# Performance work log

Hardware: AMD Instinct MI355X
Metric: run time of the kernel (lower is better)

The kernel has to match this reference:

```python
import jax, jax.numpy as jnp
import numpy as np

B, L, HID = 2, 2048, 512
NUM_HEADS = 8
HEAD_DIM = HID // NUM_HEADS
GAP_ROWS = 33   # num_time_gap_buckets + 1
DUR_ROWS = 17   # num_duration_buckets + 1
NEG = -1e9      # finite stand-in for -inf (grad-safe, masked probs ~0)


def setup_inputs() -> dict:
    key = jax.random.key(0)
    ks = jax.random.split(key, 16)
    s = 1.0 / np.sqrt(HID)
    x = jax.random.normal(ks[0], (B, L, HID), dtype=jnp.float32)
    attention_mask = jax.random.randint(ks[1], (B, L), 0, 2, dtype=jnp.int32)
    time_gap_bucket_ids = jax.random.randint(ks[2], (B, L), 0, GAP_ROWS, dtype=jnp.int32)
    duration_bucket_ids = jax.random.randint(ks[3], (B, L), 0, DUR_ROWS, dtype=jnp.int32)
    Wq = jax.random.normal(ks[4], (HID, HID), dtype=jnp.float32) * s
    bq = jnp.zeros((HID,), jnp.float32)
    Wk = jax.random.normal(ks[5], (HID, HID), dtype=jnp.float32) * s
    bk = jnp.zeros((HID,), jnp.float32)
    Wv = jax.random.normal(ks[6], (HID, HID), dtype=jnp.float32) * s
    bv = jnp.zeros((HID,), jnp.float32)
    Wo = jax.random.normal(ks[7], (HID, HID), dtype=jnp.float32) * s
    bo = jnp.zeros((HID,), jnp.float32)
    # bias tables: padding_idx=0 row kept at zero, rest random for a meaningful test
    gap_emb = jax.random.normal(ks[8], (GAP_ROWS, NUM_HEADS), dtype=jnp.float32) * 0.1
    gap_emb = gap_emb.at[0].set(0.0)
    dur_emb = jax.random.normal(ks[9], (DUR_ROWS, NUM_HEADS), dtype=jnp.float32) * 0.1
    dur_emb = dur_emb.at[0].set(0.0)
    return dict(x=x, attention_mask=attention_mask,
                time_gap_bucket_ids=time_gap_bucket_ids,
                duration_bucket_ids=duration_bucket_ids,
                Wq=Wq, bq=bq, Wk=Wk, bk=bk, Wv=Wv, bv=bv, Wo=Wo, bo=bo,
                gap_emb=gap_emb, dur_emb=dur_emb)


def reference(x, attention_mask, time_gap_bucket_ids, duration_bucket_ids,
              Wq, bq, Wk, bk, Wv, bv, Wo, bo, gap_emb, dur_emb):
    b, l, hid = x.shape
    h, d = NUM_HEADS, HEAD_DIM
    def split_heads(t):  # (B,L,HID) -> (B,h,L,d)
        return t.reshape(b, l, h, d).transpose(0, 2, 1, 3)
    Q = split_heads(x @ Wq + bq)
    K = split_heads(x @ Wk + bk)
    V = split_heads(x @ Wv + bv)
    scores = jnp.einsum('bhqd,bhkd->bhqk', Q, K) / jnp.sqrt(jnp.float32(d))
    # relative time-gap bias: (B,L,L) bucket lookup -> (B,h,L,L)
    rel = jnp.abs(time_gap_bucket_ids[:, :, None] - time_gap_bucket_ids[:, None, :])
    rel = jnp.clip(rel, 0, GAP_ROWS - 1)
    gap_bias = gap_emb[rel]                       # (B,L,L,h)
    scores = scores + gap_bias.transpose(0, 3, 1, 2)
    # per-key duration bias: (B,L,h) -> (B,h,1,L)
    dur_bias = dur_emb[duration_bucket_ids]       # (B,L,h)
    scores = scores + dur_bias.transpose(0, 2, 1)[:, :, None, :]
    pad = (attention_mask == 0)[:, None, None, :]  # (B,1,1,L) over keys
    scores = jnp.where(pad, NEG, scores)
    attn = jax.nn.softmax(scores, axis=-1)
    out = jnp.einsum('bhqk,bhkd->bhqd', attn, V)
    out = out.transpose(0, 2, 1, 3).reshape(b, l, hid)
    return out @ Wo + bo
```

## Files before the change

### kernel.cpp

```cpp
#include <hip/hip_runtime.h>
#include <cmath>

typedef unsigned short u16;
typedef unsigned int   u32;
typedef __attribute__((ext_vector_type(2))) unsigned uintx2;
typedef __attribute__((ext_vector_type(4))) float    floatx4;
typedef __attribute__((ext_vector_type(4))) unsigned uintx4;
typedef __attribute__((ext_vector_type(8))) __bf16   bf16x8;

#define MFMA16(a, b, c) __builtin_amdgcn_mfma_f32_16x16x32_bf16((a), (b), (c), 0, 0, 0)

__device__ __forceinline__ u16 f2bf(float f) {
    union { float f; u32 u; } v; v.f = f;
    u32 u = v.u;
    return (u16)((u + 0x7FFFu + ((u >> 16) & 1u)) >> 16);
}

__device__ __forceinline__ bf16x8 ld_frag(const u16* p) {
    uintx4 t = *(const uintx4*)p;
    return __builtin_bit_cast(bf16x8, t);
}

#if __has_builtin(__builtin_amdgcn_exp2f)
#define EXP2F(x) __builtin_amdgcn_exp2f(x)
#else
#define EXP2F(x) exp2f(x)
#endif

typedef __attribute__((address_space(3))) unsigned       lds_u32;
typedef __attribute__((address_space(1))) const unsigned glb_u32;
__device__ __forceinline__ void gl_lds16(const void* g, void* l) {
    __builtin_amdgcn_global_load_lds((glb_u32*)(uintptr_t)g, (lds_u32*)(uintptr_t)l, 16, 0, 0);
}

#define DRAIN() asm volatile("s_waitcnt vmcnt(0)" ::: "memory")

#define LOG2E   1.4426950408889634f
#define QSCALE  0.18033688011112043f

__global__ __launch_bounds__(256) void prep_kernel(
        const float* __restrict__ x, const int* __restrict__ gap_ids,
        const int* __restrict__ dur_ids, const int* __restrict__ amask,
        const float* __restrict__ gap_emb, const float* __restrict__ dur_emb,
        const float* __restrict__ Wq, const float* __restrict__ Wk,
        const float* __restrict__ Wv, const float* __restrict__ Wo,
        u16* __restrict__ Xb, u16* __restrict__ Qe, u16* __restrict__ Ke,
        u16* __restrict__ WqT, u16* __restrict__ WkT,
        u16* __restrict__ WvT, u16* __restrict__ WoT) {
    __shared__ u16 T[64][72];
    int bid = blockIdx.x, tid = threadIdx.x;
    if (bid < 1024) {
        int idx = bid * 256 + tid;
        const float* src = x + (size_t)idx * 8;
        uintx4 o;
        o.x = f2bf(src[0]) | ((u32)f2bf(src[1]) << 16);
        o.y = f2bf(src[2]) | ((u32)f2bf(src[3]) << 16);
        o.z = f2bf(src[4]) | ((u32)f2bf(src[5]) << 16);
        o.w = f2bf(src[6]) | ((u32)f2bf(src[7]) << 16);
        *(uintx4*)(Xb + (size_t)idx * 8) = o;
    } else if (bid < 2048) {
        int ri = (bid - 1024) * 32 + (tid >> 3);
        int l = ri & 2047;
        int b = ri >> 14;
        int ch = tid & 7;
        int gq = gap_ids[b * 2048 + l];
        u16 lg = f2bf(LOG2E);
        u16 vals[8];
        for (int e = 0; e < 8; e++) {
            int j = ch * 8 + e;
            vals[e] = (j == gq || j == 33) ? lg : (u16)0;
        }
        *(uintx4*)(Qe + (size_t)ri * 128 + (8 + ch) * 8) = *(uintx4*)vals;
    } else if (bid < 3072) {
        int ri = (bid - 2048) * 32 + (tid >> 3);
        int bh = ri >> 11, l = ri & 2047;
        int b = bh >> 3, h = bh & 7;
        int ch = tid & 7;
        int gk = gap_ids[b * 2048 + l];
        int did = dur_ids[b * 2048 + l];
        int msk = amask[b * 2048 + l];
        float kval = msk ? dur_emb[did * 8 + h] : -1e9f;
        u16 vals[8];
        for (int e = 0; e < 8; e++) {
            int j = ch * 8 + e;
            float v;
            if (j <= 32) { int d = j - gk; d = d < 0 ? -d : d; v = gap_emb[d * 8 + h]; }
            else if (j == 33) v = kval;
            else v = 0.f;
            vals[e] = f2bf(v);
        }
        int phys = 8 | (ch ^ (l & 7));
        *(uintx4*)(Ke + (size_t)ri * 128 + phys * 8) = *(uintx4*)vals;
    } else {
        int bid2 = bid - 3072;
        int mat = bid2 >> 6, t8 = bid2 & 63;
        int n0 = (t8 & 7) * 64, k0 = (t8 >> 3) * 64;
        const float* W = (mat == 0) ? Wq : (mat == 1) ? Wk : (mat == 2) ? Wv : Wo;
        u16* WT = (mat == 0) ? WqT : (mat == 1) ? WkT : (mat == 2) ? WvT : WoT;
        int r = tid >> 4, cq = tid & 15;
        for (int rr = 0; rr < 4; rr++) {
            int row = r + rr * 16;
            floatx4 s = *(const floatx4*)&W[(size_t)(k0 + row) * 512 + n0 + cq * 4];
            T[cq * 4 + 0][row] = f2bf(s.x);
            T[cq * 4 + 1][row] = f2bf(s.y);
            T[cq * 4 + 2][row] = f2bf(s.z);
            T[cq * 4 + 3][row] = f2bf(s.w);
        }
        __syncthreads();
        for (int p = 0; p < 2; p++) {
            int idx = p * 256 + tid;
            int c = idx >> 3, ch = idx & 7;
            *(uintx4*)&WT[(size_t)(n0 + c) * 512 + k0 + ch * 8] = *(const uintx4*)&T[c][ch * 8];
        }
    }
}

__global__ __launch_bounds__(256) void gemm_qkv(
        const u16* __restrict__ Xb,
        const u16* __restrict__ WqT, const u16* __restrict__ WkT, const u16* __restrict__ WvT,
        const float* __restrict__ bq, const float* __restrict__ bk, const float* __restrict__ bv,
        u16* __restrict__ Qe, u16* __restrict__ Ke, u16* __restrict__ Vt) {
    __shared__ u16 smem[2][12288];

    int tid = threadIdx.x;
    int m0 = blockIdx.x * 128;
    int gy = blockIdx.y;
    int mat = gy >> 3, hh = gy & 7;
    int ncol0 = hh * 64;
    const u16* Bt = (mat == 0) ? WqT : (mat == 1) ? WkT : WvT;
    const float* bias = (mat == 0) ? bq : (mat == 1) ? bk : bv;

    int lane = tid & 63, w = tid >> 6, lo = lane & 15, hi = lane >> 4;
    int wm = w >> 1, wn = w & 1;
    floatx4 acc[4][2] = {};

#define QSTAGE(KB, BUF) do {                                                            \
        int k0_ = (KB) * 64;                                                            \
        for (int it = 0; it < 4; it++) {                                                \
            int c = it * 256 + tid;                                                     \
            int row = c >> 3, ch = c & 7;                                               \
            gl_lds16((const char*)Xb + ((size_t)(m0 + row) * 512 + k0_) * 2 + ch * 16,  \
                     (char*)(smem[BUF]) + c * 16);                                      \
        }                                                                               \
        for (int it = 0; it < 2; it++) {                                                \
            int c = it * 256 + tid;                                                     \
            int row = c >> 3, ch = c & 7;                                               \
            gl_lds16((const char*)Bt + ((size_t)(ncol0 + row) * 512 + k0_) * 2 + ch * 16,\
                     (char*)(smem[BUF] + 8192) + c * 16);                               \
        }                                                                               \
    } while (0)

    QSTAGE(0, 0);
    for (int kb = 0; kb < 8; kb++) {
        DRAIN();
        __syncthreads();
        if (kb + 1 < 8) QSTAGE(kb + 1, (kb + 1) & 1);
        const u16* As = smem[kb & 1];
        const u16* Bs = smem[kb & 1] + 8192;
        for (int s = 0; s < 2; s++) {
            bf16x8 a[4], b[2];
            for (int i = 0; i < 4; i++)
                a[i] = ld_frag(&As[(64 * wm + 16 * i + lo) * 64 + s * 32 + hi * 8]);
            for (int j = 0; j < 2; j++)
                b[j] = ld_frag(&Bs[(32 * wn + 16 * j + lo) * 64 + s * 32 + hi * 8]);
            for (int i = 0; i < 4; i++)
                for (int j = 0; j < 2; j++)
                    acc[i][j] = MFMA16(a[i], b[j], acc[i][j]);
        }
    }
#undef QSTAGE

    int bb = m0 >> 11, l0 = m0 & 2047;
    __syncthreads();

    if (mat < 2) {
        u16* Ot = smem[0];
        for (int j = 0; j < 2; j++) {
            int col = 32 * wn + 16 * j + lo;
            float bval = bias[ncol0 + col];
            for (int i = 0; i < 4; i++) {
                int row = 64 * wm + 16 * i + 4 * hi;
                for (int r = 0; r < 4; r++) {
                    float v = acc[i][j][r] + bval;
                    if (mat == 0) v *= QSCALE;
                    Ot[(row + r) * 72 + col] = f2bf(v);
                }
            }
        }
        __syncthreads();
        for (int p = 0; p < 4; p++) {
            int cc = p * 256 + tid;
            int row = cc >> 3, ch = cc & 7;
            int lrow = l0 + row;
            size_t rowi = (size_t)(bb * 8 + hh) * 2048 + lrow;
            int ch2 = (mat == 1) ? (ch ^ (lrow & 7)) : ch;
            u16* dstp = (mat == 0) ? Qe : Ke;
            *(uintx4*)(dstp + rowi * 128 + ch2 * 8) = *(const uintx4*)(Ot + row * 72 + ch * 8);
        }
    } else {
        u16* Ot = smem[0];
        for (int j = 0; j < 2; j++) {
            int dc = 32 * wn + 16 * j + lo;
            float bval = bias[ncol0 + dc];
            for (int i = 0; i < 4; i++) {
                int row = 64 * wm + 16 * i + 4 * hi;
                for (int r = 0; r < 4; r++)
                    Ot[dc * 136 + row + r] = f2bf(acc[i][j][r] + bval);
            }
        }
        __syncthreads();
        for (int p = 0; p < 4; p++) {
            int cc4 = p * 256 + tid;
            int dc = cc4 >> 4, c16 = cc4 & 15;
            int g64 = c16 >> 3, phys = c16 & 7;
            int mlog = phys ^ (dc & 7);
            int g = mlog >> 2, q = mlog & 3;
            int base = g64 * 64 + 32 * g + 4 * q;
            uintx2 lo4 = *(const uintx2*)(Ot + dc * 136 + base);
            uintx2 hi4 = *(const uintx2*)(Ot + dc * 136 + base + 16);
            uintx4 t; t.x = lo4.x; t.y = lo4.y; t.z = hi4.x; t.w = hi4.y;
            size_t dst = ((size_t)(bb * 8 + hh) * 64 + dc) * 2048 + l0 + g64 * 64 + phys * 8;
            *(uintx4*)(Vt + dst) = t;
        }
    }
}

__global__ __launch_bounds__(256, 3) void flash_attn(
        const u16* __restrict__ Qe, const u16* __restrict__ Ke, const u16* __restrict__ Vt,
        float* __restrict__ Opart, float* __restrict__ Lpart) {
    __shared__ u16 Ks[2][64 * 128];
    __shared__ u16 Vs[2][64 * 64];

    int tid = threadIdx.x, lane = tid & 63, w = tid >> 6, lo = lane & 15, hi = lane >> 4;
    int qt2 = blockIdx.x, bh = blockIdx.y, sp = blockIdx.z;
    int sw = lo & 7;

    bf16x8 bq_[2][4];
    for (int g = 0; g < 2; g++) {
        size_t qrow = ((size_t)bh * 2048 + qt2 * 128 + g * 64 + 16 * w + lo) * 128;
        for (int kc = 0; kc < 4; kc++) bq_[g][kc] = ld_frag(&Qe[qrow + kc * 32 + hi * 8]);
    }

    floatx4 O[2][4] = {};
    floatx4 Lacc[2] = {};
    uintx4 onesu; onesu.x = 0x3F803F80u; onesu.y = 0x3F803F80u; onesu.z = 0x3F803F80u; onesu.w = 0x3F803F80u;
    bf16x8 ones = __builtin_bit_cast(bf16x8, onesu);

    const u16* KeB = Ke + (size_t)bh * 2048 * 128;
    const u16* VtB = Vt + (size_t)bh * 64 * 2048;

    int kbeg = sp * 16, kend = kbeg + 16;

#define STAGE(KT, BUF) do {                                                        \
        int k0_ = (KT) * 64;                                                       \
        const char* gk_ = (const char*)(KeB + (size_t)k0_ * 128);                  \
        char* lk_ = (char*)Ks[BUF];                                                \
        for (int r2 = 0; r2 < 4; r2++)                                             \
            gl_lds16(gk_ + r2 * 4096 + tid * 16, lk_ + r2 * 4096 + tid * 16);      \
        for (int p2 = 0; p2 < 2; p2++) {                                           \
            int c_ = p2 * 256 + tid;                                               \
            int row_ = c_ >> 3, ch_ = c_ & 7;                                      \
            gl_lds16((const char*)(VtB + (size_t)row_ * 2048 + k0_) + ch_ * 16,    \
                     (char*)Vs[BUF] + c_ * 16);                                    \
        }                                                                          \
    } while (0)

    int cur = 0;
    STAGE(kbeg, 0);
    for (int kt = kbeg; kt < kend; kt++) {
        DRAIN();
        __syncthreads();
        if (kt + 1 < kend) STAGE(kt + 1, cur ^ 1);

        const u16* Ksc = Ks[cur];
        const u16* Vsc = Vs[cur];

        floatx4 sf[2][4] = {};
        for (int t = 0; t < 4; t++) {
            const u16* krow = &Ksc[(16 * t + lo) * 128];
            for (int kc = 0; kc < 4; kc++) {
                int cc = kc * 4 + hi;
                int pc = (cc & 8) | ((cc & 7) ^ sw);
                bf16x8 a = ld_frag(&krow[pc * 8]);
                sf[0][t] = MFMA16(a, bq_[0][kc], sf[0][t]);
                sf[1][t] = MFMA16(a, bq_[1][kc], sf[1][t]);
            }
        }

        bf16x8 af[2][2];
        for (int g = 0; g < 2; g++) {
            u32 pk[4][2];
            for (int t = 0; t < 4; t++) {
                float p0 = EXP2F(sf[g][t][0]);
                float p1 = EXP2F(sf[g][t][1]);
                float p2 = EXP2F(sf[g][t][2]);
                float p3 = EXP2F(sf[g][t][3]);
                u32 u0 = __builtin_bit_cast(u32, p0) + 0x8000u;
                u32 u1 = __builtin_bit_cast(u32, p1) + 0x8000u;
                u32 u2 = __builtin_bit_cast(u32, p2) + 0x8000u;
                u32 u3 = __builtin_bit_cast(u32, p3) + 0x8000u;
                pk[t][0] = __builtin_amdgcn_perm(u1, u0, 0x07060302);
                pk[t][1] = __builtin_amdgcn_perm(u3, u2, 0x07060302);
            }
            for (int tp = 0; tp < 2; tp++) {
                uintx4 av;
                av.x = pk[2 * tp][0]; av.y = pk[2 * tp][1];
                av.z = pk[2 * tp + 1][0]; av.w = pk[2 * tp + 1][1];
                af[g][tp] = __builtin_bit_cast(bf16x8, av);
            }
        }

        for (int tp = 0; tp < 2; tp++) {
            Lacc[0] = MFMA16(af[0][tp], ones, Lacc[0]);
            Lacc[1] = MFMA16(af[1][tp], ones, Lacc[1]);
            for (int u = 0; u < 4; u++) {
                const u16* vrow = &Vsc[(16 * u + lo) * 64];
                int m = (4 * tp + hi) ^ sw;
                bf16x8 bv = ld_frag(&vrow[m * 8]);
                O[0][u] = MFMA16(af[0][tp], bv, O[0][u]);
                O[1][u] = MFMA16(af[1][tp], bv, O[1][u]);
            }
        }
        cur ^= 1;
    }
#undef STAGE

    for (int g = 0; g < 2; g++) {
        int qt = 2 * qt2 + g;
        size_t obase = (((size_t)sp * 16 + bh) * 32 + qt) * 4096;
        for (int u = 0; u < 4; u++)
            for (int r = 0; r < 4; r++)
                Opart[obase + (size_t)(16 * w + 4 * hi + r) * 64 + 16 * u + lo] = O[g][u][r];
        if (lo == 0) {
            size_t lbase = (((size_t)sp * 16 + bh) * 32 + qt) * 64;
            for (int r = 0; r < 4; r++) Lpart[lbase + 16 * w + 4 * hi + r] = Lacc[g][r];
        }
    }
}

__global__ __launch_bounds__(256) void combine_kernel(const float* __restrict__ Opart,
                                                      const float* __restrict__ Lpart,
                                                      u16* __restrict__ Ob) {
    int idx = blockIdx.x * 256 + threadIdx.x;
    int d4 = idx & 15;
    int q = (idx >> 4) & 2047;
    int bh = idx >> 15;
    int qt = q >> 6, qr = q & 63;
    size_t b0 = ((size_t)bh * 32 + qt) * 4096 + qr * 64 + d4 * 4;
    floatx4 o0 = *(const floatx4*)&Opart[b0];
    floatx4 o1 = *(const floatx4*)&Opart[b0 + 2097152];
    size_t lb = ((size_t)bh * 32 + qt) * 64 + qr;
    float rl = 1.0f / (Lpart[lb] + Lpart[lb + 32768]);
    uintx2 pk2;
    pk2.x = f2bf((o0.x + o1.x) * rl) | ((u32)f2bf((o0.y + o1.y) * rl) << 16);
    pk2.y = f2bf((o0.z + o1.z) * rl) | ((u32)f2bf((o0.w + o1.w) * rl) << 16);
    int bb = bh >> 3, h = bh & 7;
    *(uintx2*)&Ob[((size_t)(bb * 2048 + q)) * 512 + h * 64 + d4 * 4] = pk2;
}

__global__ __launch_bounds__(256) void gemm_out(
        const u16* __restrict__ Ob, const u16* __restrict__ WoT,
        const float* __restrict__ bo, float* __restrict__ out) {
    __shared__ u16 smem[2][8192];
    int tid = threadIdx.x;
    int m0 = blockIdx.x * 64;
    int n0 = blockIdx.y * 64;
    int lane = tid & 63, w = tid >> 6, lo = lane & 15, hi = lane >> 4;
    floatx4 acc[4] = {};

#define OSTAGE(KB, BUF) do {                                                            \
        int k0_ = (KB) * 64;                                                            \
        for (int it = 0; it < 2; it++) {                                                \
            int c = it * 256 + tid;                                                     \
            int row = c >> 3, ch = c & 7;                                               \
            gl_lds16((const char*)Ob + ((size_t)(m0 + row) * 512 + k0_) * 2 + ch * 16,  \
                     (char*)(smem[BUF]) + c * 16);                                      \
        }                                                                               \
        for (int it = 0; it < 2; it++) {                                                \
            int c = it * 256 + tid;                                                     \
            int row = c >> 3, ch = c & 7;                                               \
            gl_lds16((const char*)WoT + ((size_t)(n0 + row) * 512 + k0_) * 2 + ch * 16, \
                     (char*)(smem[BUF] + 4096) + c * 16);                               \
        }                                                                               \
    } while (0)

    OSTAGE(0, 0);
    for (int kb = 0; kb < 8; kb++) {
        DRAIN();
        __syncthreads();
        if (kb + 1 < 8) OSTAGE(kb + 1, (kb + 1) & 1);
        const u16* As = smem[kb & 1];
        const u16* Bs = smem[kb & 1] + 4096;
        for (int s = 0; s < 2; s++) {
            bf16x8 a = ld_frag(&As[(16 * w + lo) * 64 + s * 32 + hi * 8]);
            for (int t = 0; t < 4; t++) {
                bf16x8 b = ld_frag(&Bs[(16 * t + lo) * 64 + s * 32 + hi * 8]);
                acc[t] = MFMA16(a, b, acc[t]);
            }
        }
    }
#undef OSTAGE

    for (int t = 0; t < 4; t++) {
        int n = n0 + 16 * t + lo;
        float bval = bo[n];
        for (int r = 0; r < 4; r++) {
            int mrow = m0 + 16 * w + 4 * hi + r;
            out[(size_t)mrow * 512 + n] = acc[t][r] + bval;
        }
    }
}

extern "C" void kernel_launch(void* const* d_in, const int* in_sizes, int n_in,
                              void* d_out, int out_size, void* d_ws, size_t ws_size,
                              hipStream_t stream) {
    const float* x     = (const float*)d_in[0];
    const int*   amask = (const int*)d_in[1];
    const int*   gids  = (const int*)d_in[2];
    const int*   dids  = (const int*)d_in[3];
    const float* Wq    = (const float*)d_in[4];
    const float* bq    = (const float*)d_in[5];
    const float* Wk    = (const float*)d_in[6];
    const float* bk    = (const float*)d_in[7];
    const float* Wv    = (const float*)d_in[8];
    const float* bv    = (const float*)d_in[9];
    const float* Wo    = (const float*)d_in[10];
    const float* bo    = (const float*)d_in[11];
    const float* gap_emb = (const float*)d_in[12];
    const float* dur_emb = (const float*)d_in[13];
    float* out = (float*)d_out;

    char* ws = (char*)d_ws;
    u16*   Qe    = (u16*)(ws + 0);
    u16*   Ke    = (u16*)(ws + 8388608);
    u16*   Vt    = (u16*)(ws + 16777216);
    float* Opart = (float*)(ws + 20971520);
    float* Lpart = (float*)(ws + 37748736);
    u16*   Ob    = (u16*)(ws + 38010880);
    u16*   WoT   = (u16*)(ws + 42205184);
    u16*   Xb    = (u16*)(ws + 20971520);
    u16*   WqT   = (u16*)(ws + 25165824);
    u16*   WkT   = (u16*)(ws + 25690112);
    u16*   WvT   = (u16*)(ws + 26214400);

    hipLaunchKernelGGL(prep_kernel, dim3(3328), dim3(256), 0, stream,
                       x, gids, dids, amask, gap_emb, dur_emb,
                       Wq, Wk, Wv, Wo, Xb, Qe, Ke, WqT, WkT, WvT, WoT);
    hipLaunchKernelGGL(gemm_qkv, dim3(32, 24), dim3(256), 0, stream,
                       Xb, WqT, WkT, WvT, bq, bk, bv, Qe, Ke, Vt);
    hipLaunchKernelGGL(flash_attn, dim3(16, 16, 2), dim3(256), 0, stream,
                       Qe, Ke, Vt, Opart, Lpart);
    hipLaunchKernelGGL(combine_kernel, dim3(2048), dim3(256), 0, stream,
                       Opart, Lpart, Ob);
    hipLaunchKernelGGL(gemm_out, dim3(64, 8), dim3(256), 0, stream,
                       Ob, WoT, bo, out);
}
```

Before: 141.9 us.

## Widen QKV GEMM tile to 128 columns and store attention partials in bf16

```diff
diff --git a/kernel.cpp b/kernel.cpp
--- a/kernel.cpp
+++ b/kernel.cpp
@@ -14,6 +14,12 @@
     union { float f; u32 u; } v; v.f = f;
     u32 u = v.u;
     return (u16)((u + 0x7FFFu + ((u >> 16) & 1u)) >> 16);
+}
+__device__ __forceinline__ float bfhi2f(u32 u) {
+    return __builtin_bit_cast(float, u & 0xFFFF0000u);
+}
+__device__ __forceinline__ float bflo2f(u32 u) {
+    return __builtin_bit_cast(float, u << 16);
 }
 
 __device__ __forceinline__ bf16x8 ld_frag(const u16* p) {
@@ -120,19 +126,19 @@
         const u16* __restrict__ WqT, const u16* __restrict__ WkT, const u16* __restrict__ WvT,
         const float* __restrict__ bq, const float* __restrict__ bk, const float* __restrict__ bv,
         u16* __restrict__ Qe, u16* __restrict__ Ke, u16* __restrict__ Vt) {
-    __shared__ u16 smem[2][12288];
+    __shared__ u16 smem[2][16384];
 
     int tid = threadIdx.x;
     int m0 = blockIdx.x * 128;
     int gy = blockIdx.y;
-    int mat = gy >> 3, hh = gy & 7;
-    int ncol0 = hh * 64;
+    int mat = gy >> 2, hp = gy & 3;
+    int ncol0 = hp * 128;
     const u16* Bt = (mat == 0) ? WqT : (mat == 1) ? WkT : WvT;
     const float* bias = (mat == 0) ? bq : (mat == 1) ? bk : bv;
 
     int lane = tid & 63, w = tid >> 6, lo = lane & 15, hi = lane >> 4;
     int wm = w >> 1, wn = w & 1;
-    floatx4 acc[4][2] = {};
+    floatx4 acc[4][4] = {};
 
 #define QSTAGE(KB, BUF) do {                                                            \
         int k0_ = (KB) * 64;                                                            \
@@ -142,7 +148,7 @@
             gl_lds16((const char*)Xb + ((size_t)(m0 + row) * 512 + k0_) * 2 + ch * 16,  \
                      (char*)(smem[BUF]) + c * 16);                                      \
         }                                                                               \
-        for (int it = 0; it < 2; it++) {                                                \
+        for (int it = 0; it < 4; it++) {                                                \
             int c = it * 256 + tid;                                                     \
             int row = c >> 3, ch = c & 7;                                               \
             gl_lds16((const char*)Bt + ((size_t)(ncol0 + row) * 512 + k0_) * 2 + ch * 16,\
@@ -158,13 +164,13 @@
         const u16* As = smem[kb & 1];
         const u16* Bs = smem[kb & 1] + 8192;
         for (int s = 0; s < 2; s++) {
-            bf16x8 a[4], b[2];
+            bf16x8 a[4], b[4];
             for (int i = 0; i < 4; i++)
                 a[i] = ld_frag(&As[(64 * wm + 16 * i + lo) * 64 + s * 32 + hi * 8]);
-            for (int j = 0; j < 2; j++)
-                b[j] = ld_frag(&Bs[(32 * wn + 16 * j + lo) * 64 + s * 32 + hi * 8]);
+            for (int j = 0; j < 4; j++)
+                b[j] = ld_frag(&Bs[(64 * wn + 16 * j + lo) * 64 + s * 32 + hi * 8]);
             for (int i = 0; i < 4; i++)
-                for (int j = 0; j < 2; j++)
+                for (int j = 0; j < 4; j++)
                     acc[i][j] = MFMA16(a[i], b[j], acc[i][j]);
         }
     }
@@ -174,52 +180,56 @@
     __syncthreads();
 
     if (mat < 2) {
-        u16* Ot = smem[0];
-        for (int j = 0; j < 2; j++) {
-            int col = 32 * wn + 16 * j + lo;
-            float bval = bias[ncol0 + col];
+        u16* Ot = &smem[0][0];
+        for (int j = 0; j < 4; j++) {
+            int c64 = 16 * j + lo;
+            float bval = bias[ncol0 + 64 * wn + c64];
             for (int i = 0; i < 4; i++) {
                 int row = 64 * wm + 16 * i + 4 * hi;
                 for (int r = 0; r < 4; r++) {
                     float v = acc[i][j][r] + bval;
                     if (mat == 0) v *= QSCALE;
-                    Ot[(row + r) * 72 + col] = f2bf(v);
+                    Ot[(row + r) * 144 + wn * 72 + c64] = f2bf(v);
                 }
             }
         }
         __syncthreads();
-        for (int p = 0; p < 4; p++) {
+        for (int p = 0; p < 8; p++) {
             int cc = p * 256 + tid;
-            int row = cc >> 3, ch = cc & 7;
+            int row = cc >> 4, hcb = cc & 15;
+            int h2 = hcb >> 3, ch = hcb & 7;
             int lrow = l0 + row;
-            size_t rowi = (size_t)(bb * 8 + hh) * 2048 + lrow;
+            size_t rowi = (size_t)(bb * 8 + 2 * hp + h2) * 2048 + lrow;
             int ch2 = (mat == 1) ? (ch ^ (lrow & 7)) : ch;
             u16* dstp = (mat == 0) ? Qe : Ke;
-            *(uintx4*)(dstp + rowi * 128 + ch2 * 8) = *(const uintx4*)(Ot + row * 72 + ch * 8);
+            *(uintx4*)(dstp + rowi * 128 + ch2 * 8) =
+                *(const uintx4*)(Ot + row * 144 + h2 * 72 + ch * 8);
         }
     } else {
-        u16* Ot = smem[0];
-        for (int j = 0; j < 2; j++) {
-            int dc = 32 * wn + 16 * j + lo;
-            float bval = bias[ncol0 + dc];
+        u16* Ot = &smem[0][0];
+        for (int j = 0; j < 4; j++) {
+            int dcs = 64 * wn + 16 * j + lo;
+            float bval = bias[ncol0 + dcs];
             for (int i = 0; i < 4; i++) {
                 int row = 64 * wm + 16 * i + 4 * hi;
                 for (int r = 0; r < 4; r++)
-                    Ot[dc * 136 + row + r] = f2bf(acc[i][j][r] + bval);
-            }
-        }
-        __syncthreads();
-        for (int p = 0; p < 4; p++) {
+                    Ot[dcs * 136 + row + r] = f2bf(acc[i][j][r] + bval);
+            }
+        }
+        __syncthreads();
+        for (int p = 0; p < 8; p++) {
             int cc4 = p * 256 + tid;
-            int dc = cc4 >> 4, c16 = cc4 & 15;
+            int dcs = cc4 >> 4, c16 = cc4 & 15;
             int g64 = c16 >> 3, phys = c16 & 7;
+            int h2 = dcs >> 6, dc = dcs & 63;
             int mlog = phys ^ (dc & 7);
             int g = mlog >> 2, q = mlog & 3;
             int base = g64 * 64 + 32 * g + 4 * q;
-            uintx2 lo4 = *(const uintx2*)(Ot + dc * 136 + base);
-            uintx2 hi4 = *(const uintx2*)(Ot + dc * 136 + base + 16);
+            uintx2 lo4 = *(const uintx2*)(Ot + dcs * 136 + base);
+            uintx2 hi4 = *(const uintx2*)(Ot + dcs * 136 + base + 16);
             uintx4 t; t.x = lo4.x; t.y = lo4.y; t.z = hi4.x; t.w = hi4.y;
-            size_t dst = ((size_t)(bb * 8 + hh) * 64 + dc) * 2048 + l0 + g64 * 64 + phys * 8;
+            size_t dst = ((size_t)(bb * 8 + 2 * hp + h2) * 64 + dc) * 2048
+                         + l0 + g64 * 64 + phys * 8;
             *(uintx4*)(Vt + dst) = t;
         }
     }
@@ -227,7 +237,7 @@
 
 __global__ __launch_bounds__(256, 3) void flash_attn(
         const u16* __restrict__ Qe, const u16* __restrict__ Ke, const u16* __restrict__ Vt,
-        float* __restrict__ Opart, float* __restrict__ Lpart) {
+        u16* __restrict__ Opart, float* __restrict__ Lpart) {
     __shared__ u16 Ks[2][64 * 128];
     __shared__ u16 Vs[2][64 * 64];
 
@@ -330,7 +340,8 @@
         size_t obase = (((size_t)sp * 16 + bh) * 32 + qt) * 4096;
         for (int u = 0; u < 4; u++)
             for (int r = 0; r < 4; r++)
-                Opart[obase + (size_t)(16 * w + 4 * hi + r) * 64 + 16 * u + lo] = O[g][u][r];
+                Opart[obase + (size_t)(16 * w + 4 * hi + r) * 64 + 16 * u + lo] =
+                    f2bf(O[g][u][r]);
         if (lo == 0) {
             size_t lbase = (((size_t)sp * 16 + bh) * 32 + qt) * 64;
             for (int r = 0; r < 4; r++) Lpart[lbase + 16 * w + 4 * hi + r] = Lacc[g][r];
@@ -338,7 +349,7 @@
     }
 }
 
-__global__ __launch_bounds__(256) void combine_kernel(const float* __restrict__ Opart,
+__global__ __launch_bounds__(256) void combine_kernel(const u16* __restrict__ Opart,
                                                       const float* __restrict__ Lpart,
                                                       u16* __restrict__ Ob) {
     int idx = blockIdx.x * 256 + threadIdx.x;
@@ -347,13 +358,17 @@
     int bh = idx >> 15;
     int qt = q >> 6, qr = q & 63;
     size_t b0 = ((size_t)bh * 32 + qt) * 4096 + qr * 64 + d4 * 4;
-    floatx4 o0 = *(const floatx4*)&Opart[b0];
-    floatx4 o1 = *(const floatx4*)&Opart[b0 + 2097152];
+    uintx2 a0 = *(const uintx2*)&Opart[b0];
+    uintx2 a1 = *(const uintx2*)&Opart[b0 + 2097152];
     size_t lb = ((size_t)bh * 32 + qt) * 64 + qr;
     float rl = 1.0f / (Lpart[lb] + Lpart[lb + 32768]);
+    float s0 = bflo2f(a0.x) + bflo2f(a1.x);
+    float s1 = bfhi2f(a0.x) + bfhi2f(a1.x);
+    float s2 = bflo2f(a0.y) + bflo2f(a1.y);
+    float s3 = bfhi2f(a0.y) + bfhi2f(a1.y);
     uintx2 pk2;
-    pk2.x = f2bf((o0.x + o1.x) * rl) | ((u32)f2bf((o0.y + o1.y) * rl) << 16);
-    pk2.y = f2bf((o0.z + o1.z) * rl) | ((u32)f2bf((o0.w + o1.w) * rl) << 16);
+    pk2.x = f2bf(s0 * rl) | ((u32)f2bf(s1 * rl) << 16);
+    pk2.y = f2bf(s2 * rl) | ((u32)f2bf(s3 * rl) << 16);
     int bb = bh >> 3, h = bh & 7;
     *(uintx2*)&Ob[((size_t)(bb * 2048 + q)) * 512 + h * 64 + d4 * 4] = pk2;
 }
@@ -434,10 +449,10 @@
     u16*   Qe    = (u16*)(ws + 0);
     u16*   Ke    = (u16*)(ws + 8388608);
     u16*   Vt    = (u16*)(ws + 16777216);
-    float* Opart = (float*)(ws + 20971520);
-    float* Lpart = (float*)(ws + 37748736);
-    u16*   Ob    = (u16*)(ws + 38010880);
-    u16*   WoT   = (u16*)(ws + 42205184);
+    u16*   Opart = (u16*)(ws + 20971520);
+    float* Lpart = (float*)(ws + 29360128);
+    u16*   Ob    = (u16*)(ws + 29622272);
+    u16*   WoT   = (u16*)(ws + 33816576);
     u16*   Xb    = (u16*)(ws + 20971520);
     u16*   WqT   = (u16*)(ws + 25165824);
     u16*   WkT   = (u16*)(ws + 25690112);
@@ -446,7 +461,7 @@
     hipLaunchKernelGGL(prep_kernel, dim3(3328), dim3(256), 0, stream,
                        x, gids, dids, amask, gap_emb, dur_emb,
                        Wq, Wk, Wv, Wo, Xb, Qe, Ke, WqT, WkT, WvT, WoT);
-    hipLaunchKernelGGL(gemm_qkv, dim3(32, 24), dim3(256), 0, stream,
+    hipLaunchKernelGGL(gemm_qkv, dim3(32, 12), dim3(256), 0, stream,
                        Xb, WqT, WkT, WvT, bq, bk, bv, Qe, Ke, Vt);
     hipLaunchKernelGGL(flash_attn, dim3(16, 16, 2), dim3(256), 0, stream,
                        Qe, Ke, Vt, Opart, Lpart);
```

Measured after the change: 140.8 us. No clear change (-0.8%).
